# Kernel tuning notes

Hardware: AMD Instinct MI355X
Metric: run time of the kernel (lower is better)

Reference implementation:

```python
import jax, jax.numpy as jnp
import numpy as np

SIGMA = 4.0
KSIZE = 2 * int(4.0 * SIGMA + 0.5) + 1  # 33, as in AnomalyMapGenerator
IMAGE_SIZE = (224, 224)


def _gaussian_kernel1d(ksize, sigma):
    x = jnp.arange(ksize, dtype=jnp.float32) - ksize // 2
    g = jnp.exp(-(x * x) / (2.0 * sigma * sigma))
    return g / jnp.sum(g)


def _gaussian_blur2d(x):
    # x: [B, 1, H, W]; kornia-style GaussianBlur2d with reflect padding
    g = _gaussian_kernel1d(KSIZE, SIGMA)
    k2 = jnp.outer(g, g)[None, None]  # [1,1,K,K]
    pad = KSIZE // 2
    xp = jnp.pad(x, ((0, 0), (0, 0), (pad, pad), (pad, pad)), mode='reflect')
    return jax.lax.conv_general_dilated(xp, k2, (1, 1), 'VALID')


def _cdist(a, b):
    # Euclidean distance matrix [Na, Nb] via the expanded quadratic form
    d2 = (jnp.sum(a * a, axis=1)[:, None]
          + jnp.sum(b * b, axis=1)[None, :]
          - 2.0 * (a @ b.T))
    return jnp.sqrt(jnp.maximum(d2, 1e-12))


def setup_inputs() -> dict:
    key = jax.random.key(0)
    k1, k2 = jax.random.split(key)
    B, H, W, C, M = 16, 28, 28, 128, 16384
    embedding = jax.random.normal(k1, (B * H * W, C), dtype=jnp.float32)
    memory_bank = jax.random.normal(k2, (M, C), dtype=jnp.float32)
    return {
        'embedding': embedding,
        'memory_bank': memory_bank,
        'batch_size': B,
        'width': W,
        'height': H,
        'num_neighbors': 9,
    }


def reference(embedding, memory_bank, batch_size, width, height, num_neighbors):
    N, C = embedding.shape
    # 1-NN search: [N, M] distance matrix
    dists = _cdist(embedding, memory_bank)
    locations_flat = jnp.argmin(dists, axis=1)                      # [N]
    patch_scores_flat = jnp.take_along_axis(
        dists, locations_flat[:, None], axis=1)[:, 0]                # [N]
    patch_scores = patch_scores_flat.reshape(batch_size, -1)        # [B, HW]
    locations = locations_flat.reshape(batch_size, -1)              # [B, HW]

    # compute_anomaly_score (softmax-reweighted max patch score)
    brange = jnp.arange(batch_size)
    max_patches = jnp.argmax(patch_scores, axis=1)                  # [B]
    score = patch_scores[brange, max_patches]                       # s* per image
    nn_index = locations[brange, max_patches]                       # [B]
    nn_sample = memory_bank[nn_index]                               # [B, C]
    d_nn = _cdist(nn_sample, memory_bank)                           # [B, M]
    _, support = jax.lax.top_k(-d_nn, num_neighbors)                # [B, k]
    max_feats = embedding.reshape(batch_size, -1, C)[brange, max_patches]  # [B, C]
    support_feats = memory_bank[support]                            # [B, k, C]
    d = jnp.sqrt(jnp.maximum(
        jnp.sum((max_feats[:, None, :] - support_feats) ** 2, axis=-1), 1e-12))  # [B, k]
    weights = 1.0 - jax.nn.softmax(d, axis=1)[:, 0]
    pred_score = weights * score                                    # [B]

    # anomaly map: nearest interpolate [B,1,w,h] -> IMAGE_SIZE, then blur
    pmap = patch_scores.reshape(batch_size, 1, width, height)
    rows = jnp.arange(IMAGE_SIZE[0]) * width // IMAGE_SIZE[0]
    cols = jnp.arange(IMAGE_SIZE[1]) * height // IMAGE_SIZE[1]
    up = pmap[:, :, rows][:, :, :, cols]                            # [B,1,224,224]
    anomaly_map = _gaussian_blur2d(up)
    return anomaly_map, pred_score
```

## Files before the change

kernel.cpp:

```cpp
#include <hip/hip_runtime.h>
#include <math.h>

#define C 128
#define BIAS 256.0f

typedef __attribute__((ext_vector_type(8))) short short8;
typedef __attribute__((ext_vector_type(4))) float f32x4;
typedef __attribute__((ext_vector_type(4))) unsigned int uint4v;
typedef unsigned short u16;
typedef unsigned int u32;
typedef unsigned long long u64;

static __device__ __forceinline__ u16 f2bf(float f) {
  unsigned int u = __builtin_bit_cast(unsigned int, f);
  unsigned int r = (u + 0x7fffu + ((u >> 16) & 1u)) >> 16;
  return (u16)r;
}

static __device__ __forceinline__ float bf2f(short s) {
  return __uint_as_float(((u32)(u16)s) << 16);
}

static __device__ __forceinline__ void gload_lds16(const void* g, void* l) {
  __builtin_amdgcn_global_load_lds(
      (const __attribute__((address_space(1))) unsigned int*)g,
      (__attribute__((address_space(3))) unsigned int*)l, 16, 0, 0);
}

__global__ __launch_bounds__(256) void prep_kernel(
    const float* __restrict__ emb, const float* __restrict__ bank,
    u16* __restrict__ Abf, u16* __restrict__ Bbf, float* __restrict__ anorm,
    float* __restrict__ bnorm, u64* __restrict__ packed, int* __restrict__ cnt,
    int N, int M) {
  const int tid = threadIdx.x;
  const int chunk = blockIdx.x * 256 + tid;
  const int total = (N + M) * (C / 8);
  if (chunk >= total) return;
  if (chunk < N) packed[chunk] = ~0ull;
  if (chunk < 16) cnt[chunk] = 0;
  const int gr = chunk >> 4;
  const int co = (chunk & 15) * 8;
  const float* src;
  u16* dst;
  float* ndst;
  int r;
  float sc;
  if (gr < N) { src = emb; dst = Abf; ndst = anorm; r = gr; sc = 1.0f; }
  else { src = bank; dst = Bbf; ndst = bnorm; r = gr - N; sc = -2.0f; }
  const float* p = src + (size_t)r * C + co;
  float4 v0 = *(const float4*)p;
  float4 v1 = *(const float4*)(p + 4);
  u16 o[8] = {f2bf(sc * v0.x), f2bf(sc * v0.y), f2bf(sc * v0.z),
              f2bf(sc * v0.w), f2bf(sc * v1.x), f2bf(sc * v1.y),
              f2bf(sc * v1.z), f2bf(sc * v1.w)};
  *(uint4v*)(dst + (size_t)r * C + co) = *(const uint4v*)o;
  float s = v0.x * v0.x + v0.y * v0.y + v0.z * v0.z + v0.w * v0.w +
            v1.x * v1.x + v1.y * v1.y + v1.z * v1.z + v1.w * v1.w;
#pragma unroll
  for (int m = 1; m <= 8; m <<= 1) s += __shfl_xor(s, m, 64);
  if ((tid & 15) == 0) ndst[r] = s;
}

__global__ __launch_bounds__(256, 4) void nn_mfma(
    const u16* __restrict__ Abf, const u16* __restrict__ Bbf,
    const float* __restrict__ bnorm, const float* __restrict__ anorm,
    u64* __restrict__ packed, int N, int M) {
  __shared__ short Bs[2][8192];
  const int tid = threadIdx.x;
  const int lane = tid & 63;
  const int w = tid >> 6;
  const int lr = lane & 15, kg = lane >> 4;
  const int bid = blockIdx.x;
  const int sub = bid & 15;
  const int row0 = (bid >> 4) * 128;
  const int j0base = (sub & 7) * (M >> 3) + (sub >> 3) * (M >> 4);

  int soff[4];
#pragma unroll
  for (int q = 0; q < 4; ++q) {
    const int r = q * 16 + (tid >> 4);
    const int c = (((tid & 15) * 16) ^ ((r & 7) << 4)) >> 1;
    soff[q] = r * C + c;
  }

#define STAGE(bufi, jj)                                                     \
  do {                                                                      \
    const u16* gsrc = Bbf + (size_t)(jj) * C;                               \
    _Pragma("unroll") for (int q = 0; q < 4; ++q)                           \
        gload_lds16(gsrc + soff[q], &Bs[bufi][q * 2048 + w * 512]);         \
  } while (0)

  short8 af[2][4];
  {
    const u16* pa = Abf + (size_t)(row0 + w * 32 + lr) * C + kg * 8;
#pragma unroll
    for (int fi = 0; fi < 2; ++fi)
#pragma unroll
      for (int k = 0; k < 4; ++k)
        af[fi][k] = *(const short8*)(pa + fi * 16 * C + k * 32);
  }

  u32 minv[8];
#pragma unroll
  for (int s = 0; s < 8; ++s) minv[s] = 0xFFFFFFFFu;

  STAGE(0, j0base);

  const float* bnp = bnorm + j0base + lr;
  float bnc[4], bnn[4];
#pragma unroll
  for (int fj = 0; fj < 4; ++fj) bnc[fj] = bnp[fj * 16] + BIAS;

  __syncthreads();

  int j0 = j0base;
  for (int t = 0; t < 16; ++t) {
    const int buf = t & 1;
    if (t < 15) {
      STAGE(buf ^ 1, j0 + 64);
#pragma unroll
      for (int fj = 0; fj < 4; ++fj)
        bnn[fj] = bnp[(t + 1) * 64 + fj * 16] + BIAS;
    }

    f32x4 acc[2][4];
#pragma unroll
    for (int fi = 0; fi < 2; ++fi)
#pragma unroll
      for (int fj = 0; fj < 4; ++fj)
        acc[fi][fj] = (f32x4){bnc[fj], bnc[fj], bnc[fj], bnc[fj]};

    const short* bsb = &Bs[buf][0];
    const int cxor = (lr & 7) << 3;
#pragma unroll
    for (int k = 0; k < 4; ++k) {
      const int ko = (k * 32 + kg * 8) ^ cxor;
      short8 bf[4];
#pragma unroll
      for (int fj = 0; fj < 4; ++fj)
        bf[fj] = *(const short8*)&bsb[(fj * 16 + lr) * C + ko];
#pragma unroll
      for (int fi = 0; fi < 2; ++fi)
#pragma unroll
        for (int fj = 0; fj < 4; ++fj)
          acc[fi][fj] = __builtin_amdgcn_mfma_f32_16x16x32_bf16(
              af[fi][k], bf[fj], acc[fi][fj], 0, 0, 0);
    }

#pragma unroll
    for (int fj = 0; fj < 4; ++fj) {
      const u32 col = (u32)(j0 + fj * 16 + lr);
#pragma unroll
      for (int fi = 0; fi < 2; ++fi) {
#pragma unroll
        for (int r = 0; r < 4; ++r) {
          u32 key = (__float_as_uint(acc[fi][fj][r]) & 0xFFFFC000u) | col;
          const int s = fi * 4 + r;
          minv[s] = key < minv[s] ? key : minv[s];
        }
      }
    }
#pragma unroll
    for (int fj = 0; fj < 4; ++fj) bnc[fj] = bnn[fj];
    __syncthreads();
    j0 += 64;
  }
#undef STAGE

#pragma unroll
  for (int s = 0; s < 8; ++s) {
    u32 k = minv[s];
#pragma unroll
    for (int m = 1; m <= 8; m <<= 1) {
      u32 ok = (u32)__shfl_xor((int)k, m, 64);
      k = ok < k ? ok : k;
    }
    if (lr == 0) {
      const int row = row0 + w * 32 + (s >> 2) * 16 + kg * 4 + (s & 3);
      const u32 col = k & 0x3FFFu;
      const float vm = __uint_as_float(k & 0xFFFFC000u);
      float d2 = fmaxf(anorm[row] + (vm - BIAS), 0.0f);
      u64 pk = ((u64)__float_as_uint(d2) << 32) | col;
      atomicMin(&packed[row], pk);
    }
  }
}

__global__ __launch_bounds__(256) void post_kernel(
    const u16* __restrict__ Bbf, const float* __restrict__ bnorm,
    const u64* __restrict__ packed, const float* __restrict__ emb,
    const float* __restrict__ Bk, float* __restrict__ score,
    int* __restrict__ maxrow, float* __restrict__ cvals,
    int* __restrict__ cidx, int* __restrict__ cnt, float* __restrict__ pred,
    float* __restrict__ out, int M) {
  const int b = blockIdx.y;
  const int tid = threadIdx.x;
  __shared__ float vecf[C];
  __shared__ float sv[256];
  __shared__ int si[256];
  __shared__ int sl[256];
  __shared__ float wv[288];
  __shared__ int wi[288];
  __shared__ int sp[256];
  __shared__ int sup[9];
  __shared__ float ds[9];

  if (blockIdx.x >= 32) {
    const int q = blockIdx.x - 32;
    float* g = vecf;
    float (*rows)[28] = (float(*)[28]) & sv[0];
    float (*gvs)[5] = (float(*)[5]) & wv[0];
    const int rc0 = q < 2 ? 0 : (q > 25 ? 23 : q - 2);
    if (tid < 33) {
      float d = (float)tid - 16.0f;
      g[tid] = expf(-(d * d) * (1.0f / 32.0f));
    }
    if (tid < 140) {
      const int i = tid / 28, cc = tid - i * 28;
      u64 p = packed[(size_t)b * 784 + (rc0 + i) * 28 + cc];
      float d2 = __uint_as_float((unsigned)(p >> 32));
      rows[i][cc] = sqrtf(fmaxf(d2, 1e-12f));
    }
    __syncthreads();
    if (tid == 0) {
      float s = 0.0f;
      for (int t = 0; t < 33; ++t) s += g[t];
      ds[0] = 1.0f / (s * s);
    }
    if (tid < 40) {
      const int dy = tid / 5, i = tid - dy * 5;
      const int y = q * 8 + dy;
      float acc = 0.0f;
      for (int t = 0; t < 33; ++t) {
        int yy = y + t - 16;
        yy = yy < 0 ? -yy : (yy > 223 ? 446 - yy : yy);
        acc += ((yy >> 3) - rc0 == i) ? g[t] : 0.0f;
      }
      gvs[dy][i] = acc;
    }
    __syncthreads();
    if (tid < 224) {
      float hacc[5];
#pragma unroll
      for (int i = 0; i < 5; ++i) hacc[i] = 0.0f;
      for (int s = 0; s < 33; ++s) {
        int xx = tid + s - 16;
        xx = xx < 0 ? -xx : (xx > 223 ? 446 - xx : xx);
        const int cs = xx >> 3;
        const float gs_ = g[s];
#pragma unroll
        for (int i = 0; i < 5; ++i) hacc[i] += gs_ * rows[i][cs];
      }
      const float ginv = ds[0];
#pragma unroll
      for (int dy = 0; dy < 8; ++dy) {
        float acc = 0.0f;
#pragma unroll
        for (int i = 0; i < 5; ++i) acc += gvs[dy][i] * hacc[i];
        out[((size_t)b * 224 + q * 8 + dy) * 224 + tid] = acc * ginv;
      }
    }
    return;
  }

  const int c = blockIdx.x;

  {
    float bv = -INFINITY;
    int bi_ = 0x7fffffff, bl = 0;
    for (int i = tid; i < 784; i += 256) {
      u64 p = packed[(size_t)b * 784 + i];
      float v = __uint_as_float((unsigned)(p >> 32));
      if (v > bv) { bv = v; bi_ = i; bl = (int)(unsigned)p; }
    }
    sv[tid] = bv; si[tid] = bi_; sl[tid] = bl;
    __syncthreads();
    for (int s = 128; s > 0; s >>= 1) {
      if (tid < s) {
        if (sv[tid + s] > sv[tid] ||
            (sv[tid + s] == sv[tid] && si[tid + s] < si[tid])) {
          sv[tid] = sv[tid + s]; si[tid] = si[tid + s]; sl[tid] = sl[tid + s];
        }
      }
      __syncthreads();
    }
  }
  const int nn = sl[0];
  if (c == 0 && tid == 0) {
    score[b] = sqrtf(fmaxf(sv[0], 1e-12f));
    maxrow[b] = b * 784 + si[0];
  }
  __syncthreads();

  if (tid < 16) {
    short8 v = ((const short8*)(Bbf + (size_t)nn * C))[tid];
#pragma unroll
    for (int e = 0; e < 8; ++e) vecf[tid * 8 + e] = bf2f(v[e]);
  }
  __syncthreads();
  const float nnorm = bnorm[nn];
  const int j0 = c * (M >> 5);
  float rv[2];
  int rj[2];
#pragma unroll
  for (int q = 0; q < 2; ++q) {
    const int j = j0 + q * 256 + tid;
    const short8* br = (const short8*)(Bbf + (size_t)j * C);
    float dot = 0.0f;
#pragma unroll
    for (int kc = 0; kc < 16; ++kc) {
      short8 v = br[kc];
      float4 w0 = *(const float4*)&vecf[kc * 8];
      float4 w1 = *(const float4*)&vecf[kc * 8 + 4];
      dot += bf2f(v[0]) * w0.x + bf2f(v[1]) * w0.y + bf2f(v[2]) * w0.z +
             bf2f(v[3]) * w0.w + bf2f(v[4]) * w1.x + bf2f(v[5]) * w1.y +
             bf2f(v[6]) * w1.z + bf2f(v[7]) * w1.w;
    }
    rv[q] = nnorm + bnorm[j] - 0.5f * dot;
    rj[q] = j;
  }
  for (int s9 = 0; s9 < 9; ++s9) {
    float bv = INFINITY;
    int bj = 0x7fffffff;
#pragma unroll
    for (int q = 0; q < 2; ++q)
      if (rv[q] < bv) { bv = rv[q]; bj = rj[q]; }
    sv[tid] = bv; si[tid] = bj;
    __syncthreads();
    for (int s = 128; s > 0; s >>= 1) {
      if (tid < s) {
        if (sv[tid + s] < sv[tid] ||
            (sv[tid + s] == sv[tid] && si[tid + s] < si[tid])) {
          sv[tid] = sv[tid + s]; si[tid] = si[tid + s];
        }
      }
      __syncthreads();
    }
    const int selj = si[0];
    if (tid == 0) {
      cvals[((size_t)b * 32 + c) * 9 + s9] = sv[0];
      cidx[((size_t)b * 32 + c) * 9 + s9] = selj;
    }
#pragma unroll
    for (int q = 0; q < 2; ++q)
      if (rj[q] == selj) rv[q] = INFINITY;
    __syncthreads();
  }

  if (tid == 0) {
    __threadfence();
    sl[0] = atomicAdd(&cnt[b], 1);
  }
  __syncthreads();
  if (sl[0] != 31) return;
  __threadfence();

  for (int i = tid; i < 288; i += 256) {
    wv[i] = cvals[(size_t)b * 288 + i];
    wi[i] = cidx[(size_t)b * 288 + i];
  }
  if (tid < 32)
    *(float4*)&vecf[tid * 4] =
        *(const float4*)(emb + (size_t)maxrow[b] * C + tid * 4);
  __syncthreads();
  for (int s9 = 0; s9 < 9; ++s9) {
    float bv = INFINITY;
    int bi_ = 0x7fffffff, bp = -1;
    for (int i = tid; i < 288; i += 256) {
      if (wv[i] < bv || (wv[i] == bv && wi[i] < bi_)) {
        bv = wv[i]; bi_ = wi[i]; bp = i;
      }
    }
    sv[tid] = bv; si[tid] = bi_; sp[tid] = bp;
    __syncthreads();
    for (int s = 128; s > 0; s >>= 1) {
      if (tid < s) {
        if (sv[tid + s] < sv[tid] ||
            (sv[tid + s] == sv[tid] && si[tid + s] < si[tid])) {
          sv[tid] = sv[tid + s]; si[tid] = si[tid + s]; sp[tid] = sp[tid + s];
        }
      }
      __syncthreads();
    }
    if (tid == 0) {
      sup[s9] = si[0];
      wv[sp[0]] = INFINITY;
    }
    __syncthreads();
  }
  const int w = tid >> 6, lane = tid & 63;
  for (int s = w; s < 9; s += 4) {
    const float* br = Bk + (size_t)sup[s] * C;
    float d0 = vecf[lane * 2] - br[lane * 2];
    float d1 = vecf[lane * 2 + 1] - br[lane * 2 + 1];
    float acc = d0 * d0 + d1 * d1;
#pragma unroll
    for (int m = 1; m <= 32; m <<= 1) acc += __shfl_xor(acc, m, 64);
    if (lane == 0) ds[s] = sqrtf(fmaxf(acc, 1e-12f));
  }
  __syncthreads();
  if (tid == 0) {
    float m = ds[0];
    for (int t = 1; t < 9; ++t) m = fmaxf(m, ds[t]);
    float sum = 0.0f, e0 = 0.0f;
    for (int t = 0; t < 9; ++t) {
      float e = expf(ds[t] - m);
      sum += e;
      if (t == 0) e0 = e;
    }
    pred[b] = (1.0f - e0 / sum) * score[b];
  }
}

extern "C" void kernel_launch(void* const* d_in, const int* in_sizes, int n_in,
                              void* d_out, int out_size, void* d_ws,
                              size_t ws_size, hipStream_t stream) {
  const float* emb = (const float*)d_in[0];
  const float* bank = (const float*)d_in[1];
  const int N = in_sizes[0] / C;
  const int M = in_sizes[1] / C;
  const int B = 16;

  u16* Abf = (u16*)d_ws;
  u16* Bbf = Abf + (size_t)N * C;
  u64* packed = (u64*)(Bbf + (size_t)M * C);
  float* anorm = (float*)(packed + N);
  float* bnorm = anorm + N;
  float* score = bnorm + M;
  int* maxrow = (int*)(score + B);
  float* cvals = (float*)(maxrow + B);
  int* cidx = (int*)(cvals + B * 288);
  int* cnt = cidx + B * 288;

  float* out_map = (float*)d_out;
  float* out_pred = out_map + (size_t)B * 224 * 224;

  const int total = (N + M) * (C / 8);
  prep_kernel<<<(total + 255) / 256, 256, 0, stream>>>(
      emb, bank, Abf, Bbf, anorm, bnorm, packed, cnt, N, M);
  nn_mfma<<<(N / 128) * 16, 256, 0, stream>>>(Abf, Bbf, bnorm, anorm, packed,
                                              N, M);
  post_kernel<<<dim3(60, B), 256, 0, stream>>>(Bbf, bnorm, packed, emb, bank,
                                               score, maxrow, cvals, cidx,
                                               cnt, out_pred, out_map, M);
}
```

Baseline: 122.3 us.

## Split each block's 128x64 tile into a 2x2 wave grid of 64x32

Changes the per-wave tile from 32 rows x 64 columns to 64 rows x 32 columns, arranged as a 2x2 grid of waves. Each wave now holds 4 A fragments in registers and reads only 2 B fragments from LDS per k-step instead of 4, which halves LDS read traffic per MFMA. In exchange it doubles A-fragment registers and min-accumulators, and moves the bnorm loads into the loop without prefetching them. That may raise register pressure under the launch bound of 4 blocks per CU.

```diff
diff --git a/kernel.cpp b/kernel.cpp
--- a/kernel.cpp
+++ b/kernel.cpp
@@ -69,6 +69,7 @@
   const int tid = threadIdx.x;
   const int lane = tid & 63;
   const int w = tid >> 6;
+  const int wr = w >> 1, wc = w & 1;
   const int lr = lane & 15, kg = lane >> 4;
   const int bid = blockIdx.x;
   const int sub = bid & 15;
@@ -90,68 +91,60 @@
         gload_lds16(gsrc + soff[q], &Bs[bufi][q * 2048 + w * 512]);         \
   } while (0)
 
-  short8 af[2][4];
+  short8 af[4][4];
   {
-    const u16* pa = Abf + (size_t)(row0 + w * 32 + lr) * C + kg * 8;
-#pragma unroll
-    for (int fi = 0; fi < 2; ++fi)
+    const u16* pa = Abf + (size_t)(row0 + wr * 64 + lr) * C + kg * 8;
+#pragma unroll
+    for (int fi = 0; fi < 4; ++fi)
 #pragma unroll
       for (int k = 0; k < 4; ++k)
         af[fi][k] = *(const short8*)(pa + fi * 16 * C + k * 32);
   }
 
-  u32 minv[8];
-#pragma unroll
-  for (int s = 0; s < 8; ++s) minv[s] = 0xFFFFFFFFu;
+  u32 minv[16];
+#pragma unroll
+  for (int s = 0; s < 16; ++s) minv[s] = 0xFFFFFFFFu;
 
   STAGE(0, j0base);
-
-  const float* bnp = bnorm + j0base + lr;
-  float bnc[4], bnn[4];
-#pragma unroll
-  for (int fj = 0; fj < 4; ++fj) bnc[fj] = bnp[fj * 16] + BIAS;
-
   __syncthreads();
 
   int j0 = j0base;
   for (int t = 0; t < 16; ++t) {
     const int buf = t & 1;
-    if (t < 15) {
-      STAGE(buf ^ 1, j0 + 64);
-#pragma unroll
-      for (int fj = 0; fj < 4; ++fj)
-        bnn[fj] = bnp[(t + 1) * 64 + fj * 16] + BIAS;
-    }
-
-    f32x4 acc[2][4];
-#pragma unroll
-    for (int fi = 0; fi < 2; ++fi)
-#pragma unroll
-      for (int fj = 0; fj < 4; ++fj)
-        acc[fi][fj] = (f32x4){bnc[fj], bnc[fj], bnc[fj], bnc[fj]};
+    if (t < 15) STAGE(buf ^ 1, j0 + 64);
+
+    const float bnb0 = bnorm[j0 + wc * 32 + lr] + BIAS;
+    const float bnb1 = bnorm[j0 + wc * 32 + 16 + lr] + BIAS;
+
+    f32x4 acc[4][2];
+#pragma unroll
+    for (int fi = 0; fi < 4; ++fi) {
+      acc[fi][0] = (f32x4){bnb0, bnb0, bnb0, bnb0};
+      acc[fi][1] = (f32x4){bnb1, bnb1, bnb1, bnb1};
+    }
 
     const short* bsb = &Bs[buf][0];
     const int cxor = (lr & 7) << 3;
 #pragma unroll
     for (int k = 0; k < 4; ++k) {
       const int ko = (k * 32 + kg * 8) ^ cxor;
-      short8 bf[4];
-#pragma unroll
-      for (int fj = 0; fj < 4; ++fj)
-        bf[fj] = *(const short8*)&bsb[(fj * 16 + lr) * C + ko];
-#pragma unroll
-      for (int fi = 0; fi < 2; ++fi)
-#pragma unroll
-        for (int fj = 0; fj < 4; ++fj)
-          acc[fi][fj] = __builtin_amdgcn_mfma_f32_16x16x32_bf16(
-              af[fi][k], bf[fj], acc[fi][fj], 0, 0, 0);
-    }
-
-#pragma unroll
-    for (int fj = 0; fj < 4; ++fj) {
-      const u32 col = (u32)(j0 + fj * 16 + lr);
-#pragma unroll
-      for (int fi = 0; fi < 2; ++fi) {
+      short8 bf0 = *(const short8*)&bsb[(wc * 32 + lr) * C + ko];
+      short8 bf1 = *(const short8*)&bsb[(wc * 32 + 16 + lr) * C + ko];
+#pragma unroll
+      for (int fi = 0; fi < 4; ++fi)
+        acc[fi][0] = __builtin_amdgcn_mfma_f32_16x16x32_bf16(
+            af[fi][k], bf0, acc[fi][0], 0, 0, 0);
+#pragma unroll
+      for (int fi = 0; fi < 4; ++fi)
+        acc[fi][1] = __builtin_amdgcn_mfma_f32_16x16x32_bf16(
+            af[fi][k], bf1, acc[fi][1], 0, 0, 0);
+    }
+
+#pragma unroll
+    for (int fj = 0; fj < 2; ++fj) {
+      const u32 col = (u32)(j0 + wc * 32 + fj * 16 + lr);
+#pragma unroll
+      for (int fi = 0; fi < 4; ++fi) {
 #pragma unroll
         for (int r = 0; r < 4; ++r) {
           u32 key = (__float_as_uint(acc[fi][fj][r]) & 0xFFFFC000u) | col;
@@ -160,15 +153,13 @@
         }
       }
     }
-#pragma unroll
-    for (int fj = 0; fj < 4; ++fj) bnc[fj] = bnn[fj];
     __syncthreads();
     j0 += 64;
   }
 #undef STAGE
 
 #pragma unroll
-  for (int s = 0; s < 8; ++s) {
+  for (int s = 0; s < 16; ++s) {
     u32 k = minv[s];
 #pragma unroll
     for (int m = 1; m <= 8; m <<= 1) {
@@ -176,7 +167,7 @@
       k = ok < k ? ok : k;
     }
     if (lr == 0) {
-      const int row = row0 + w * 32 + (s >> 2) * 16 + kg * 4 + (s & 3);
+      const int row = row0 + wr * 64 + (s >> 2) * 16 + kg * 4 + (s & 3);
       const u32 col = k & 0x3FFFu;
       const float vm = __uint_as_float(k & 0xFFFFC000u);
       float d2 = fmaxf(anorm[row] + (vm - BIAS), 0.0f);
```

Measured after the change: 151.7 us. 24.0% more time.
